# Optimization experiments

Measured on AMD Instinct MI355X. Metric: run time of the kernel, lower is better.

The kernel has to match this reference:

```python
import jax, jax.numpy as jnp
import numpy as np

B, H, S, DK = 2, 16, 2048, 64
NEG = jnp.float32(-10000.0)


def setup_inputs() -> dict:
    key = jax.random.key(0)
    kq, kk, kv, km = jax.random.split(key, 4)
    query = jax.random.normal(kq, (B, H, S, DK), dtype=jnp.float32)
    k_ = jax.random.normal(kk, (B, H, S, DK), dtype=jnp.float32)
    value = jax.random.normal(kv, (B, H, S, DK), dtype=jnp.float32)
    mask = (jax.random.uniform(km, (B, 1, S, S)) > 0.5).astype(jnp.float32)
    return {"query": query, "key": k_, "value": value, "mask": mask, "d_k": DK}


def reference(query, key, value, mask, d_k):
    # scores: [B,H,S,S]
    scale = jnp.float32(1.0 / np.sqrt(d_k))
    scores = jnp.einsum('bhqd,bhkd->bhqk', query, key) * scale * mask
    # non-standard masking: keep only strictly positive masked scores
    scores = jnp.where(scores > 0, scores, NEG)
    attn = jax.nn.softmax(scores, axis=-1)
    return jnp.einsum('bhqk,bhkd->bhqd', attn, value)
```

## Files before the change

### kernel.cpp

```cpp
#include <hip/hip_runtime.h>
#include <math.h>

#define S_LEN 2048
#define D_KV  64
#define BQ    128
#define BK    64
#define NT    (S_LEN / BK)

typedef __attribute__((ext_vector_type(8)))  short bh8;
typedef __attribute__((ext_vector_type(4)))  float fx4;
typedef __attribute__((ext_vector_type(16))) float fx16;
typedef __attribute__((ext_vector_type(4)))  unsigned int u32x4;
typedef __attribute__((ext_vector_type(2)))  unsigned int u32x2;

__device__ __forceinline__ unsigned cvt2(float a, float b) {
    unsigned r;
    asm("v_cvt_pk_bf16_f32 %0, %1, %2" : "=v"(r) : "v"(a), "v"(b));
    return r;
}
__device__ __forceinline__ void swap32(unsigned &d, unsigned &s) {
    asm("v_permlane32_swap_b32 %0, %1" : "+v"(d), "+v"(s));
}
__device__ __forceinline__ float exp2_fast(float x) {
    float r;
    asm("v_exp_f32 %0, %1" : "=v"(r) : "v"(x));
    return r;
}
__device__ __forceinline__ int swz(int row, int byteoff) {
    return (row << 7) + (byteoff ^ ((row & 7) << 4));
}

__global__ __launch_bounds__(256)
void pack_mask(const float* __restrict__ M, unsigned long long* __restrict__ BM)
{
    const size_t i = (size_t)blockIdx.x * 256 + threadIdx.x;
    const float v = M[i];
    const unsigned long long bits = __ballot(v > 0.5f);
    if ((threadIdx.x & 63) == 0) {
        const size_t g = i >> 6;
        const int col64 = (int)(g & 31);
        const int row   = (int)((g >> 5) & 2047);
        const int b     = (int)(g >> 16);
        BM[((size_t)b * 32 + col64) * 2048 + row] = bits;
    }
}

__global__ __launch_bounds__(256, 3)
void attn_fwd(const float* __restrict__ Qg, const float* __restrict__ Kg,
              const float* __restrict__ Vg,
              const unsigned long long* __restrict__ BMg,
              float* __restrict__ Og)
{
    __shared__ __align__(16) char smem[16384];
    short* kb = (short*)smem;
    short* vb = (short*)(smem + 8192);

    const int tid  = threadIdx.x;
    const int lane = tid & 63;
    const int wave = tid >> 6;
    const int lq   = lane & 31;
    const int hf   = lane >> 5;

    const int flat = blockIdx.x + (int)gridDim.x * blockIdx.y;
    const int nsw  = (flat & 7) * 64 + (flat >> 3);
    const int qt = nsw & 15;
    const int bh = nsw >> 4;
    const int b  = bh >> 4;

    const int qbase = qt * BQ + wave * 32;

    const float* Kp = Kg + (size_t)bh * S_LEN * D_KV;
    const float* Vp = Vg + (size_t)bh * S_LEN * D_KV;
    const float* Qp = Qg + ((size_t)bh * S_LEN + qbase) * D_KV;
    const unsigned long long* BMp = BMg + (size_t)b * 32 * 2048 + qbase + lq;

    const float QS = 0.125f * 1.44269504f;
    bh8 qf[4];
#pragma unroll
    for (int ks = 0; ks < 4; ++ks) {
        const float* src = Qp + lq * D_KV + ks * 16 + hf * 8;
        fx4 a0 = *(const fx4*)src;
        fx4 a1 = *(const fx4*)(src + 4);
        u32x4 q4 = { cvt2(a0[0] * QS, a0[1] * QS),
                     cvt2(a0[2] * QS, a0[3] * QS),
                     cvt2(a1[0] * QS, a1[1] * QS),
                     cvt2(a1[2] * QS, a1[3] * QS) };
        qf[ks] = __builtin_bit_cast(bh8, q4);
    }

    const int krow = tid >> 2;
    const int kcol = (tid & 3) << 2;
    const int vd0  = (tid >> 4) << 2;
    const int vk0  = (tid & 15) << 2;

    fx16 o0 = {}, o1 = {};
    float lsum = 0.f;
    fx4 kreg[4], vreg[4];

    auto issue = [&](int kt) {
#pragma unroll
        for (int i = 0; i < 4; ++i)
            kreg[i] = *(const fx4*)(Kp + (size_t)(kt + krow) * D_KV + kcol + 16 * i);
#pragma unroll
        for (int i = 0; i < 4; ++i)
            vreg[i] = *(const fx4*)(Vp + (size_t)(kt + vk0 + i) * D_KV + vd0);
    };

    issue(0);

#pragma unroll 1
    for (int t = 0; t < NT; ++t) {
        const unsigned long long bm = BMp[(size_t)t * 2048];

#pragma unroll
        for (int i = 0; i < 4; ++i) {
            u32x2 w = { cvt2(kreg[i][0], kreg[i][1]),
                        cvt2(kreg[i][2], kreg[i][3]) };
            *(u32x2*)((char*)kb + swz(krow, (kcol << 1) + 32 * i)) = w;
        }
#pragma unroll
        for (int i = 0; i < 4; ++i) {
            u32x2 w = { cvt2(vreg[0][i], vreg[1][i]),
                        cvt2(vreg[2][i], vreg[3][i]) };
            *(u32x2*)((char*)vb + swz(vd0 + i, vk0 << 1)) = w;
        }
        asm volatile("s_waitcnt lgkmcnt(0)" ::: "memory");
        __builtin_amdgcn_s_barrier();

        if (t + 1 < NT) issue((t + 1) * BK);

        fx16 st0 = {}, st1 = {};
        __builtin_amdgcn_s_setprio(1);
#pragma unroll
        for (int ks = 0; ks < 4; ++ks) {
            bh8 k0 = *(const bh8*)((char*)kb + swz(lq,      ks * 32 + hf * 16));
            bh8 k1 = *(const bh8*)((char*)kb + swz(32 + lq, ks * 32 + hf * 16));
            st0 = __builtin_amdgcn_mfma_f32_32x32x16_bf16(k0, qf[ks], st0, 0, 0, 0);
            st1 = __builtin_amdgcn_mfma_f32_32x32x16_bf16(k1, qf[ks], st1, 0, 0, 0);
        }
        __builtin_amdgcn_s_setprio(0);

        const unsigned s0 = ((unsigned)bm) >> (hf * 4);
        const unsigned s1 = ((unsigned)(bm >> 32)) >> (hf * 4);

        unsigned pkw[16];

#pragma unroll
        for (int m = 0; m < 4; ++m) {
            const unsigned bb = s0 >> (8 * m);
            float tm0 = st0[4*m+0], tm1 = st0[4*m+1];
            float tm2 = st0[4*m+2], tm3 = st0[4*m+3];
            float p0 = ((bb      & 1) && tm0 > 0.f) ? exp2_fast(tm0) : 0.f;
            float p1 = ((bb >> 1 & 1) && tm1 > 0.f) ? exp2_fast(tm1) : 0.f;
            float p2 = ((bb >> 2 & 1) && tm2 > 0.f) ? exp2_fast(tm2) : 0.f;
            float p3 = ((bb >> 3 & 1) && tm3 > 0.f) ? exp2_fast(tm3) : 0.f;
            lsum += (p0 + p1) + (p2 + p3);
            pkw[m*2+0] = cvt2(p0, p1);
            pkw[m*2+1] = cvt2(p2, p3);
        }

        __builtin_amdgcn_s_setprio(1);
#pragma unroll
        for (int vp = 0; vp < 2; ++vp) {
            unsigned w0 = pkw[vp*4+0], w1 = pkw[vp*4+1];
            unsigned w2 = pkw[vp*4+2], w3 = pkw[vp*4+3];
            swap32(w0, w2); swap32(w1, w3);
            u32x4 pq = { w0, w1, w2, w3 };
            bh8 pb = __builtin_bit_cast(bh8, pq);
            bh8 v0 = *(const bh8*)((char*)vb + swz(lq,      vp * 32 + hf * 16));
            bh8 v1 = *(const bh8*)((char*)vb + swz(32 + lq, vp * 32 + hf * 16));
            o0 = __builtin_amdgcn_mfma_f32_32x32x16_bf16(v0, pb, o0, 0, 0, 0);
            o1 = __builtin_amdgcn_mfma_f32_32x32x16_bf16(v1, pb, o1, 0, 0, 0);
        }
        __builtin_amdgcn_s_setprio(0);

#pragma unroll
        for (int m = 0; m < 4; ++m) {
            const unsigned bb = s1 >> (8 * m);
            float tm0 = st1[4*m+0], tm1 = st1[4*m+1];
            float tm2 = st1[4*m+2], tm3 = st1[4*m+3];
            float p0 = ((bb      & 1) && tm0 > 0.f) ? exp2_fast(tm0) : 0.f;
            float p1 = ((bb >> 1 & 1) && tm1 > 0.f) ? exp2_fast(tm1) : 0.f;
            float p2 = ((bb >> 2 & 1) && tm2 > 0.f) ? exp2_fast(tm2) : 0.f;
            float p3 = ((bb >> 3 & 1) && tm3 > 0.f) ? exp2_fast(tm3) : 0.f;
            lsum += (p0 + p1) + (p2 + p3);
            pkw[8 + m*2+0] = cvt2(p0, p1);
            pkw[8 + m*2+1] = cvt2(p2, p3);
        }

        __builtin_amdgcn_s_setprio(1);
#pragma unroll
        for (int vp = 2; vp < 4; ++vp) {
            unsigned w0 = pkw[vp*4+0], w1 = pkw[vp*4+1];
            unsigned w2 = pkw[vp*4+2], w3 = pkw[vp*4+3];
            swap32(w0, w2); swap32(w1, w3);
            u32x4 pq = { w0, w1, w2, w3 };
            bh8 pb = __builtin_bit_cast(bh8, pq);
            bh8 v0 = *(const bh8*)((char*)vb + swz(lq,      vp * 32 + hf * 16));
            bh8 v1 = *(const bh8*)((char*)vb + swz(32 + lq, vp * 32 + hf * 16));
            o0 = __builtin_amdgcn_mfma_f32_32x32x16_bf16(v0, pb, o0, 0, 0, 0);
            o1 = __builtin_amdgcn_mfma_f32_32x32x16_bf16(v1, pb, o1, 0, 0, 0);
        }
        __builtin_amdgcn_s_setprio(0);

        __builtin_amdgcn_s_barrier();
    }

    lsum += __shfl_xor(lsum, 32);
    const float inv = 1.0f / lsum;

    float* orow = Og + ((size_t)bh * S_LEN + qbase + lq) * D_KV;
#pragma unroll
    for (int m = 0; m < 4; ++m) {
        fx4 r0 = { o0[4*m+0]*inv, o0[4*m+1]*inv, o0[4*m+2]*inv, o0[4*m+3]*inv };
        *(fx4*)(orow + m * 8 + hf * 4) = r0;
        fx4 r1 = { o1[4*m+0]*inv, o1[4*m+1]*inv, o1[4*m+2]*inv, o1[4*m+3]*inv };
        *(fx4*)(orow + 32 + m * 8 + hf * 4) = r1;
    }
}

extern "C" void kernel_launch(void* const* d_in, const int* in_sizes, int n_in,
                              void* d_out, int out_size, void* d_ws, size_t ws_size,
                              hipStream_t stream) {
    const float* Q = (const float*)d_in[0];
    const float* K = (const float*)d_in[1];
    const float* V = (const float*)d_in[2];
    const float* M = (const float*)d_in[3];
    float*       O = (float*)d_out;
    unsigned long long* BM = (unsigned long long*)d_ws;

    pack_mask<<<dim3(32768), 256, 0, stream>>>(M, BM);

    dim3 grid(S_LEN / BQ, 32);
    attn_fwd<<<grid, 256, 0, stream>>>(Q, K, V, BM, O);
}
```

Before: 194.7 us.

## Split key range across two wave groups per block and merge partials in LDS

Each block now runs 512 threads: two groups of four waves each process half of the key sequence for the same 128 queries with separate LDS tiles, then group 1 writes its partial output and row sum to shared memory and group 0 combines and stores. This doubles the waves in flight per query tile to hide the serial key-loop latency. The mask packing kernel is rewritten so each thread builds one byte from 8 floats with vector loads instead of a ballot per element. K staging now uses 16-byte LDS stores. In exchange the block needs 36 KB of LDS and a final reduction barrier, which may limit occupancy.

```diff
diff --git a/kernel.cpp b/kernel.cpp
--- a/kernel.cpp
+++ b/kernel.cpp
@@ -5,7 +5,8 @@
 #define D_KV  64
 #define BQ    128
 #define BK    64
-#define NT    (S_LEN / BK)
+#define KHALF 1024
+#define NT    (KHALF / BK)
 
 typedef __attribute__((ext_vector_type(8)))  short bh8;
 typedef __attribute__((ext_vector_type(4)))  float fx4;
@@ -31,35 +32,45 @@
 }
 
 __global__ __launch_bounds__(256)
-void pack_mask(const float* __restrict__ M, unsigned long long* __restrict__ BM)
+void pack_mask(const float* __restrict__ M, unsigned char* __restrict__ BM)
 {
-    const size_t i = (size_t)blockIdx.x * 256 + threadIdx.x;
-    const float v = M[i];
-    const unsigned long long bits = __ballot(v > 0.5f);
-    if ((threadIdx.x & 63) == 0) {
-        const size_t g = i >> 6;
-        const int col64 = (int)(g & 31);
-        const int row   = (int)((g >> 5) & 2047);
-        const int b     = (int)(g >> 16);
-        BM[((size_t)b * 32 + col64) * 2048 + row] = bits;
-    }
-}
-
-__global__ __launch_bounds__(256, 3)
+    const int t = blockIdx.x * 256 + threadIdx.x;
+    const int bytecol = t & 7;
+    const int row     = (t >> 3) & 2047;
+    const int col64   = (t >> 14) & 31;
+    const int b       = t >> 19;
+    const float* src = M + ((size_t)b * 2048 + row) * 2048 + col64 * 64 + bytecol * 8;
+    fx4 a = *(const fx4*)src;
+    fx4 c = *(const fx4*)(src + 4);
+    unsigned bits = (a[0] > 0.5f)
+                  | ((unsigned)(a[1] > 0.5f) << 1)
+                  | ((unsigned)(a[2] > 0.5f) << 2)
+                  | ((unsigned)(a[3] > 0.5f) << 3)
+                  | ((unsigned)(c[0] > 0.5f) << 4)
+                  | ((unsigned)(c[1] > 0.5f) << 5)
+                  | ((unsigned)(c[2] > 0.5f) << 6)
+                  | ((unsigned)(c[3] > 0.5f) << 7);
+    BM[t] = (unsigned char)bits;
+}
+
+__global__ __launch_bounds__(512, 4)
 void attn_fwd(const float* __restrict__ Qg, const float* __restrict__ Kg,
               const float* __restrict__ Vg,
               const unsigned long long* __restrict__ BMg,
               float* __restrict__ Og)
 {
-    __shared__ __align__(16) char smem[16384];
-    short* kb = (short*)smem;
-    short* vb = (short*)(smem + 8192);
+    __shared__ __align__(16) char smem[36864];
 
     const int tid  = threadIdx.x;
     const int lane = tid & 63;
     const int wave = tid >> 6;
+    const int qw   = wave & 3;
+    const int kg   = wave >> 2;
     const int lq   = lane & 31;
     const int hf   = lane >> 5;
+
+    short* kb = (short*)(smem + kg * 16384);
+    short* vb = (short*)(smem + kg * 16384 + 8192);
 
     const int flat = blockIdx.x + (int)gridDim.x * blockIdx.y;
     const int nsw  = (flat & 7) * 64 + (flat >> 3);
@@ -67,12 +78,13 @@
     const int bh = nsw >> 4;
     const int b  = bh >> 4;
 
-    const int qbase = qt * BQ + wave * 32;
-
-    const float* Kp = Kg + (size_t)bh * S_LEN * D_KV;
-    const float* Vp = Vg + (size_t)bh * S_LEN * D_KV;
+    const int qbase = qt * BQ + qw * 32;
+
+    const float* Kp = Kg + ((size_t)bh * S_LEN + kg * KHALF) * D_KV;
+    const float* Vp = Vg + ((size_t)bh * S_LEN + kg * KHALF) * D_KV;
     const float* Qp = Qg + ((size_t)bh * S_LEN + qbase) * D_KV;
-    const unsigned long long* BMp = BMg + (size_t)b * 32 * 2048 + qbase + lq;
+    const unsigned long long* BMp =
+        BMg + (size_t)b * 32 * 2048 + (size_t)(kg * NT) * 2048 + qbase + lq;
 
     const float QS = 0.125f * 1.44269504f;
     bh8 qf[4];
@@ -88,19 +100,21 @@
         qf[ks] = __builtin_bit_cast(bh8, q4);
     }
 
-    const int krow = tid >> 2;
-    const int kcol = (tid & 3) << 2;
-    const int vd0  = (tid >> 4) << 2;
-    const int vk0  = (tid & 15) << 2;
+    const int stid  = tid & 255;
+    const int krow  = stid >> 2;
+    const int kcolf = (stid & 3) << 4;
+    const int vd0   = (stid >> 4) << 2;
+    const int vk0   = (stid & 15) << 2;
 
     fx16 o0 = {}, o1 = {};
     float lsum = 0.f;
     fx4 kreg[4], vreg[4];
 
     auto issue = [&](int kt) {
+        const float* ksrc = Kp + (size_t)(kt + krow) * D_KV + kcolf;
 #pragma unroll
         for (int i = 0; i < 4; ++i)
-            kreg[i] = *(const fx4*)(Kp + (size_t)(kt + krow) * D_KV + kcol + 16 * i);
+            kreg[i] = *(const fx4*)(ksrc + 4 * i);
 #pragma unroll
         for (int i = 0; i < 4; ++i)
             vreg[i] = *(const fx4*)(Vp + (size_t)(kt + vk0 + i) * D_KV + vd0);
@@ -113,10 +127,12 @@
         const unsigned long long bm = BMp[(size_t)t * 2048];
 
 #pragma unroll
-        for (int i = 0; i < 4; ++i) {
-            u32x2 w = { cvt2(kreg[i][0], kreg[i][1]),
-                        cvt2(kreg[i][2], kreg[i][3]) };
-            *(u32x2*)((char*)kb + swz(krow, (kcol << 1) + 32 * i)) = w;
+        for (int j = 0; j < 2; ++j) {
+            u32x4 w = { cvt2(kreg[2*j][0],   kreg[2*j][1]),
+                        cvt2(kreg[2*j][2],   kreg[2*j][3]),
+                        cvt2(kreg[2*j+1][0], kreg[2*j+1][1]),
+                        cvt2(kreg[2*j+1][2], kreg[2*j+1][3]) };
+            *(u32x4*)((char*)kb + swz(krow, (kcolf << 1) + 16 * j)) = w;
         }
 #pragma unroll
         for (int i = 0; i < 4; ++i) {
@@ -207,15 +223,43 @@
     }
 
     lsum += __shfl_xor(lsum, 32);
-    const float inv = 1.0f / lsum;
-
-    float* orow = Og + ((size_t)bh * S_LEN + qbase + lq) * D_KV;
-#pragma unroll
-    for (int m = 0; m < 4; ++m) {
-        fx4 r0 = { o0[4*m+0]*inv, o0[4*m+1]*inv, o0[4*m+2]*inv, o0[4*m+3]*inv };
-        *(fx4*)(orow + m * 8 + hf * 4) = r0;
-        fx4 r1 = { o1[4*m+0]*inv, o1[4*m+1]*inv, o1[4*m+2]*inv, o1[4*m+3]*inv };
-        *(fx4*)(orow + 32 + m * 8 + hf * 4) = r1;
+
+    float* scr = (float*)smem;
+    const int slot = qw * 64 + lane;
+    if (kg) {
+        float* d = scr + slot * 36;
+#pragma unroll
+        for (int i = 0; i < 4; ++i) {
+            fx4 c0 = { o0[4*i+0], o0[4*i+1], o0[4*i+2], o0[4*i+3] };
+            *(fx4*)(d + 4 * i) = c0;
+            fx4 c1 = { o1[4*i+0], o1[4*i+1], o1[4*i+2], o1[4*i+3] };
+            *(fx4*)(d + 16 + 4 * i) = c1;
+        }
+        d[32] = lsum;
+    }
+    __syncthreads();
+    if (!kg) {
+        const float* s = scr + slot * 36;
+#pragma unroll
+        for (int i = 0; i < 4; ++i) {
+            fx4 c0 = *(const fx4*)(s + 4 * i);
+            o0[4*i+0] += c0[0]; o0[4*i+1] += c0[1];
+            o0[4*i+2] += c0[2]; o0[4*i+3] += c0[3];
+            fx4 c1 = *(const fx4*)(s + 16 + 4 * i);
+            o1[4*i+0] += c1[0]; o1[4*i+1] += c1[1];
+            o1[4*i+2] += c1[2]; o1[4*i+3] += c1[3];
+        }
+        lsum += s[32];
+        const float inv = 1.0f / lsum;
+
+        float* orow = Og + ((size_t)bh * S_LEN + qbase + lq) * D_KV;
+#pragma unroll
+        for (int m = 0; m < 4; ++m) {
+            fx4 r0 = { o0[4*m+0]*inv, o0[4*m+1]*inv, o0[4*m+2]*inv, o0[4*m+3]*inv };
+            *(fx4*)(orow + m * 8 + hf * 4) = r0;
+            fx4 r1 = { o1[4*m+0]*inv, o1[4*m+1]*inv, o1[4*m+2]*inv, o1[4*m+3]*inv };
+            *(fx4*)(orow + 32 + m * 8 + hf * 4) = r1;
+        }
     }
 }
 
@@ -227,10 +271,10 @@
     const float* V = (const float*)d_in[2];
     const float* M = (const float*)d_in[3];
     float*       O = (float*)d_out;
-    unsigned long long* BM = (unsigned long long*)d_ws;
-
-    pack_mask<<<dim3(32768), 256, 0, stream>>>(M, BM);
+
+    pack_mask<<<dim3(4096), 256, 0, stream>>>(M, (unsigned char*)d_ws);
 
     dim3 grid(S_LEN / BQ, 32);
-    attn_fwd<<<grid, 256, 0, stream>>>(Q, K, V, BM, O);
-}
+    attn_fwd<<<grid, 512, 0, stream>>>(Q, K, V,
+                                       (const unsigned long long*)d_ws, O);
+}
```

After: 293.1 us. +50.5%, slower.
